# Performance work log

Measured on AMD Instinct MI355X. Metric: run time of the kernel, lower is better.

## Reference

```python
import jax, jax.numpy as jnp
import numpy as np

B, S, E, H, L = 2, 2048, 1024, 16, 64


def setup_inputs() -> dict:
    key = jax.random.key(0)
    ks = jax.random.split(key, 9)
    x = jax.random.normal(ks[0], (B, S, E), dtype=jnp.float32)
    # causal mask: 1 where attention allowed, 0 where blocked (mask==0 -> -inf)
    mask = jnp.tril(jnp.ones((1, S, S), dtype=jnp.int32))
    std = 0.02
    # per-head Linear weights stacked over heads; torch Linear stores W as [out, in]
    Wq = jax.random.normal(ks[1], (H, L, E), dtype=jnp.float32) * std
    Wk = jax.random.normal(ks[2], (H, L, E), dtype=jnp.float32) * std
    Wv = jax.random.normal(ks[3], (H, L, E), dtype=jnp.float32) * std
    bq = jax.random.normal(ks[4], (H, L), dtype=jnp.float32) * std
    bk = jax.random.normal(ks[5], (H, L), dtype=jnp.float32) * std
    bv = jax.random.normal(ks[6], (H, L), dtype=jnp.float32) * std
    Wo = jax.random.normal(ks[7], (E, H * L), dtype=jnp.float32) * std
    bo = jax.random.normal(ks[8], (E,), dtype=jnp.float32) * std
    return {"x": x, "mask": mask, "Wq": Wq, "bq": bq, "Wk": Wk, "bk": bk,
            "Wv": Wv, "bv": bv, "Wo": Wo, "bo": bo}


def reference(x, mask, Wq, bq, Wk, bk, Wv, bv, Wo, bo):
    # Q/K/V for all heads at once: [B, H, S, L]
    Q = jnp.einsum('bse,hle->bhsl', x, Wq) + bq[None, :, None, :]
    K = jnp.einsum('bse,hle->bhsl', x, Wk) + bk[None, :, None, :]
    V = jnp.einsum('bse,hle->bhsl', x, Wv) + bv[None, :, None, :]
    scale = jnp.sqrt(jnp.asarray(L, dtype=Q.dtype))
    scores = jnp.einsum('bhsl,bhtl->bhst', Q, K) / scale  # [B,H,S,S]
    scores = jnp.where(mask[:, None, :, :] == 0, -jnp.inf, scores)
    P = jax.nn.softmax(scores, axis=-1)
    O = jnp.einsum('bhst,bhtl->bhsl', P, V)  # [B,H,S,L]
    # concat heads along last dim (head order matches torch concat)
    z = jnp.transpose(O, (0, 2, 1, 3)).reshape(O.shape[0], O.shape[2], -1)
    return jnp.einsum('bsk,ek->bse', z, Wo) + bo
```

## Files before the change

### kernel.cpp

```cpp
#include <hip/hip_runtime.h>
#include <math.h>

typedef unsigned short US;
typedef __attribute__((ext_vector_type(8))) __bf16 bf16x8;
typedef __attribute__((ext_vector_type(4))) float f32x4;
typedef __attribute__((ext_vector_type(4))) unsigned short us4;

#define MFMA16(a, b, c) __builtin_amdgcn_mfma_f32_16x16x32_bf16(a, b, c, 0, 0, 0)

__device__ __forceinline__ US f2bf(float f) {
  union { float f; unsigned u; } v; v.f = f;
  unsigned r = v.u + 0x7fffu + ((v.u >> 16) & 1u);
  return (US)(r >> 16);
}
__device__ __forceinline__ float bf2f(US u) {
  union { unsigned u; float f; } v; v.u = ((unsigned)u) << 16; return v.f;
}

__device__ __forceinline__ void gload16(const void* g, void* l) {
  __builtin_amdgcn_global_load_lds(
      (const __attribute__((address_space(1))) unsigned int*)g,
      (__attribute__((address_space(3))) unsigned int*)l, 16, 0, 0);
}

__global__ __launch_bounds__(256) void convert_k(
    const float* __restrict__ x, const float* __restrict__ Wq,
    const float* __restrict__ Wk, const float* __restrict__ Wv,
    const float* __restrict__ Wo,
    US* __restrict__ xb, US* __restrict__ wqkv, US* __restrict__ wob) {
  long i = (long)blockIdx.x * blockDim.x + threadIdx.x;
  long e4 = i * 4;
  if (e4 >= 8388608L) return;
  const float* src; US* dst;
  if (e4 < 4194304L) { src = x + e4; dst = xb + e4; }
  else if (e4 < 7340032L) {
    long off = e4 - 4194304L;
    dst = wqkv + off;
    src = (off < 1048576L) ? Wq + off
        : (off < 2097152L ? Wk + (off - 1048576L) : Wv + (off - 2097152L));
  } else {
    long off = e4 - 7340032L;
    src = Wo + off; dst = wob + off;
  }
  float4 v = *(const float4*)src;
  us4 o; o.x = f2bf(v.x); o.y = f2bf(v.y); o.z = f2bf(v.z); o.w = f2bf(v.w);
  *(us4*)dst = o;
}

template <int MODE>
__global__ __launch_bounds__(256) void gemm128(
    const US* __restrict__ A, const US* __restrict__ BT,
    int K, int lda, int ldb, int N,
    const float* __restrict__ b0, const float* __restrict__ b1,
    const float* __restrict__ b2,
    US* __restrict__ oQ, US* __restrict__ oK, US* __restrict__ oV,
    float* __restrict__ oF) {
  __shared__ __align__(16) US As[128 * 32];
  __shared__ __align__(16) US Bs[128 * 32];
  const int tid = threadIdx.x, lane = tid & 63;
  const int w = tid >> 6, wr = w >> 1, wc = w & 1;
  const int m0 = blockIdx.x * 128, n0 = blockIdx.y * 128;
  f32x4 acc[4][4] = {};
  const int r0 = tid >> 2, c0 = (tid & 3) * 8;

  for (int kt = 0; kt < K; kt += 32) {
    gload16(A + (size_t)(m0 + r0) * lda + kt + c0, As + tid * 8);
    gload16(A + (size_t)(m0 + r0 + 64) * lda + kt + c0, As + (tid + 256) * 8);
    gload16(BT + (size_t)(n0 + r0) * ldb + kt + c0, Bs + tid * 8);
    gload16(BT + (size_t)(n0 + r0 + 64) * ldb + kt + c0, Bs + (tid + 256) * 8);
    __syncthreads();
    bf16x8 af[4], bfm[4];
#pragma unroll
    for (int i = 0; i < 4; ++i)
      af[i] = *(const bf16x8*)(As + (wr * 64 + i * 16 + (lane & 15)) * 32 + (lane >> 4) * 8);
#pragma unroll
    for (int j = 0; j < 4; ++j)
      bfm[j] = *(const bf16x8*)(Bs + (wc * 64 + j * 16 + (lane & 15)) * 32 + (lane >> 4) * 8);
#pragma unroll
    for (int i = 0; i < 4; ++i)
#pragma unroll
      for (int j = 0; j < 4; ++j)
        acc[i][j] = MFMA16(af[i], bfm[j], acc[i][j]);
    __syncthreads();
  }

#pragma unroll
  for (int i = 0; i < 4; ++i) {
#pragma unroll
    for (int j = 0; j < 4; ++j) {
#pragma unroll
      for (int r = 0; r < 4; ++r) {
        int m = m0 + wr * 64 + i * 16 + (lane >> 4) * 4 + r;
        int n = n0 + wc * 64 + j * 16 + (lane & 15);
        float v = acc[i][j][r];
        if (MODE == 0) {
          int bb = m >> 11, s = m & 2047;
          int sec = n >> 10, idx = n & 1023;
          int h = idx >> 6, l = idx & 63;
          size_t bhsl = (((size_t)bb * 16 + h) * 2048 + s) * 64 + l;
          if (sec == 0)      oQ[bhsl] = f2bf((v + b0[idx]) * 0.125f);
          else if (sec == 1) oK[bhsl] = f2bf(v + b1[idx]);
          else oV[(((size_t)bb * 16 + h) * 64 + l) * 2048 + s] = f2bf(v + b2[idx]);
        } else {
          oF[(size_t)m * N + n] = v + b0[n];
        }
      }
    }
  }
}

__global__ __launch_bounds__(256) void attn_k(
    const US* __restrict__ Qb, const US* __restrict__ Kb,
    const US* __restrict__ Vtb, US* __restrict__ opart,
    float2* __restrict__ mlpart) {
  __shared__ __align__(16) US Ks[64 * 64];
  __shared__ __align__(16) US Vs[64 * 64];
  __shared__ __align__(16) US Ps[4][16 * 72];
  const int tid = threadIdx.x, lane = tid & 63, w = tid >> 6;
  const int slot = blockIdx.x >> 6;
  const int qt = 31 - slot;
  const int bh = (blockIdx.x & 63) >> 1;
  const int half = blockIdx.x & 1;
  const int h0 = (qt + 2) >> 1;
  const int kstart = half ? h0 : 0;
  const int kend = half ? (qt + 1) : h0;
  const size_t pslot = (size_t)(bh * 32 + qt) * 2 + half;

  if (kstart >= kend) {
    US* op = opart + pslot * 4096;
    us4 z; z.x = 0; z.y = 0; z.z = 0; z.w = 0;
#pragma unroll
    for (int j = 0; j < 4; ++j) *(us4*)(op + tid * 16 + j * 4) = z;
    if ((lane >> 4) == 0)
      mlpart[pslot * 64 + w * 16 + lane] = make_float2(-INFINITY, 0.f);
    return;
  }

  const US* Qp = Qb + ((size_t)bh * 2048 + qt * 64) * 64;
  const char* Kbase = (const char*)(Kb + (size_t)bh * 2048 * 64);
  const char* Vbase = (const char*)(Vtb + (size_t)bh * 64 * 2048);

  const int row0 = tid >> 3, col16 = (tid & 7) * 16;
  const int row1 = row0 + 32;
  const int soff0 = (row0 * 128 + col16) ^ ((row0 & 7) << 4);
  const int soff1 = soff0 + 32 * 128;

  bf16x8 aq[2];
  {
    int qrow = w * 16 + (lane & 15);
#pragma unroll
    for (int kk = 0; kk < 2; ++kk)
      aq[kk] = *(const bf16x8*)(Qp + qrow * 64 + kk * 32 + (lane >> 4) * 8);
  }
  f32x4 o[4] = {};
  float m = -INFINITY, l = 0.f;

  int4 rk0, rk1, rv0, rv1;
#define LOADT(KT)                                                              \
  do {                                                                         \
    rk0 = *(const int4*)(Kbase + ((size_t)((KT)*64 + row0)) * 128 + col16);    \
    rk1 = *(const int4*)(Kbase + ((size_t)((KT)*64 + row1)) * 128 + col16);    \
    rv0 = *(const int4*)(Vbase + (size_t)row0 * 4096 + (KT)*128 + col16);      \
    rv1 = *(const int4*)(Vbase + (size_t)row1 * 4096 + (KT)*128 + col16);      \
  } while (0)
#define WRITET()                                                               \
  do {                                                                         \
    *(int4*)((char*)Ks + soff0) = rk0;                                         \
    *(int4*)((char*)Ks + soff1) = rk1;                                         \
    *(int4*)((char*)Vs + soff0) = rv0;                                         \
    *(int4*)((char*)Vs + soff1) = rv1;                                         \
  } while (0)

  LOADT(kstart);
  WRITET();
  __syncthreads();

  for (int kt = kstart; kt < kend; ++kt) {
    if (kt + 1 < kend) LOADT(kt + 1);

    f32x4 sc[4];
    __builtin_amdgcn_s_setprio(1);
#pragma unroll
    for (int nt = 0; nt < 4; ++nt) {
      f32x4 s = {0.f, 0.f, 0.f, 0.f};
#pragma unroll
      for (int kk = 0; kk < 2; ++kk) {
        int rr = nt * 16 + (lane & 15);
        int off = rr * 128 + kk * 64 + (lane >> 4) * 16;
        off ^= (rr & 7) << 4;
        bf16x8 bkf = *(const bf16x8*)((const char*)Ks + off);
        s = MFMA16(bkf, aq[kk], s);
      }
      sc[nt] = s;
    }
    __builtin_amdgcn_s_setprio(0);

    if (kt == qt) {
      int q_in = w * 16 + (lane & 15);
#pragma unroll
      for (int nt = 0; nt < 4; ++nt)
#pragma unroll
        for (int r = 0; r < 4; ++r) {
          int kv_in = nt * 16 + (lane >> 4) * 4 + r;
          if (kv_in > q_in) sc[nt][r] = -INFINITY;
        }
    }

    {
      float m01 = fmaxf(fmaxf(sc[0][0], sc[0][1]), fmaxf(sc[0][2], sc[0][3]));
      float m23 = fmaxf(fmaxf(sc[1][0], sc[1][1]), fmaxf(sc[1][2], sc[1][3]));
      float m45 = fmaxf(fmaxf(sc[2][0], sc[2][1]), fmaxf(sc[2][2], sc[2][3]));
      float m67 = fmaxf(fmaxf(sc[3][0], sc[3][1]), fmaxf(sc[3][2], sc[3][3]));
      float mx = fmaxf(fmaxf(m01, m23), fmaxf(m45, m67));
      mx = fmaxf(mx, __shfl_xor(mx, 16));
      mx = fmaxf(mx, __shfl_xor(mx, 32));
      float mnew = fmaxf(m, mx);
      float scale = __expf(m - mnew);
      m = mnew;
      float s0 = 0.f, s1 = 0.f, s2 = 0.f, s3 = 0.f;
#pragma unroll
      for (int nt = 0; nt < 4; ++nt) {
        float p0 = __expf(sc[nt][0] - m);
        float p1 = __expf(sc[nt][1] - m);
        float p2 = __expf(sc[nt][2] - m);
        float p3 = __expf(sc[nt][3] - m);
        sc[nt][0] = p0; sc[nt][1] = p1; sc[nt][2] = p2; sc[nt][3] = p3;
        s0 += p0; s1 += p1; s2 += p2; s3 += p3;
      }
      float ssum = (s0 + s1) + (s2 + s3);
      ssum += __shfl_xor(ssum, 16);
      ssum += __shfl_xor(ssum, 32);
      l = l * scale + ssum;
#pragma unroll
      for (int r = 0; r < 4; ++r) {
        float sr = __shfl(scale, ((lane >> 4) << 2) + r, 64);
        o[0][r] *= sr; o[1][r] *= sr; o[2][r] *= sr; o[3][r] *= sr;
      }
    }

    US* pp = &Ps[w][0];
    const int pbase = (lane & 15) * 72 + (lane >> 4) * 4;
#pragma unroll
    for (int nt = 0; nt < 4; ++nt) {
      us4 w4;
      w4.x = f2bf(sc[nt][0]); w4.y = f2bf(sc[nt][1]);
      w4.z = f2bf(sc[nt][2]); w4.w = f2bf(sc[nt][3]);
      *(us4*)(pp + pbase + nt * 16) = w4;
    }

    __builtin_amdgcn_s_setprio(1);
#pragma unroll
    for (int kk = 0; kk < 2; ++kk) {
      bf16x8 pa = *(const bf16x8*)(pp + (lane & 15) * 72 + kk * 32 + (lane >> 4) * 8);
#pragma unroll
      for (int nt = 0; nt < 4; ++nt) {
        int rr = nt * 16 + (lane & 15);
        int off = rr * 128 + kk * 64 + (lane >> 4) * 16;
        off ^= (rr & 7) << 4;
        bf16x8 bvf = *(const bf16x8*)((const char*)Vs + off);
        o[nt] = MFMA16(pa, bvf, o[nt]);
      }
    }
    __builtin_amdgcn_s_setprio(0);

    __syncthreads();
    if (kt + 1 < kend) {
      WRITET();
      __syncthreads();
    }
  }
#undef LOADT
#undef WRITET

  US* op = opart + pslot * 4096;
#pragma unroll
  for (int r = 0; r < 4; ++r) {
    int row = w * 16 + (lane >> 4) * 4 + r;
#pragma unroll
    for (int nt = 0; nt < 4; ++nt) {
      int d = nt * 16 + (lane & 15);
      op[row * 64 + d] = f2bf(o[nt][r]);
    }
  }
  if ((lane >> 4) == 0)
    mlpart[pslot * 64 + w * 16 + lane] = make_float2(m, l);
}

__global__ __launch_bounds__(256) void merge_k(
    const US* __restrict__ opart, const float2* __restrict__ mlpart,
    US* __restrict__ zb) {
  const int t = blockIdx.x;
  const int bh = t >> 5, qt = t & 31;
  const int b = bh >> 4, h = bh & 15;
  const int row = threadIdx.x >> 2;
  const int dg = (threadIdx.x & 3) * 16;
  const US* o1 = opart + ((size_t)t * 2 + 0) * 4096 + row * 64 + dg;
  const US* o2 = opart + ((size_t)t * 2 + 1) * 4096 + row * 64 + dg;
  float2 ml1 = mlpart[(t * 2 + 0) * 64 + row];
  float2 ml2 = mlpart[(t * 2 + 1) * 64 + row];
  float mm = fmaxf(ml1.x, ml2.x);
  float w1 = __expf(ml1.x - mm), w2 = __expf(ml2.x - mm);
  float li = 1.0f / (ml1.y * w1 + ml2.y * w2);
  w1 *= li; w2 *= li;
  int s = qt * 64 + row;
  US* dst = zb + ((size_t)b * 2048 + s) * 1024 + h * 64 + dg;
#pragma unroll
  for (int j = 0; j < 4; ++j) {
    us4 a = *(const us4*)(o1 + j * 4);
    us4 c = *(const us4*)(o2 + j * 4);
    us4 r;
    r.x = f2bf(bf2f(a.x) * w1 + bf2f(c.x) * w2);
    r.y = f2bf(bf2f(a.y) * w1 + bf2f(c.y) * w2);
    r.z = f2bf(bf2f(a.z) * w1 + bf2f(c.z) * w2);
    r.w = f2bf(bf2f(a.w) * w1 + bf2f(c.w) * w2);
    *(us4*)(dst + j * 4) = r;
  }
}

extern "C" void kernel_launch(void* const* d_in, const int* in_sizes, int n_in,
                              void* d_out, int out_size, void* d_ws, size_t ws_size,
                              hipStream_t stream) {
  (void)in_sizes; (void)n_in; (void)out_size; (void)ws_size;
  const float* x  = (const float*)d_in[0];
  const float* Wq = (const float*)d_in[2];
  const float* bq = (const float*)d_in[3];
  const float* Wk = (const float*)d_in[4];
  const float* bk = (const float*)d_in[5];
  const float* Wv = (const float*)d_in[6];
  const float* bv = (const float*)d_in[7];
  const float* Wo = (const float*)d_in[8];
  const float* bo = (const float*)d_in[9];
  char* ws = (char*)d_ws;
  US* xb     = (US*)(ws);
  float2* ml = (float2*)(ws);
  US* zb     = (US*)(ws + 1048576);
  US* wqkv   = (US*)(ws + 8388608);
  US* wob    = (US*)(ws + 14680064);
  US* Qb     = (US*)(ws + 16777216);
  US* Kb     = (US*)(ws + 25165824);
  US* Vtb    = (US*)(ws + 33554432);
  US* opart  = (US*)d_out;
  float* out = (float*)d_out;

  convert_k<<<dim3(8192), dim3(256), 0, stream>>>(x, Wq, Wk, Wv, Wo, xb, wqkv, wob);
  gemm128<0><<<dim3(32, 24), dim3(256), 0, stream>>>(
      xb, wqkv, 1024, 1024, 1024, 3072, bq, bk, bv, Qb, Kb, Vtb, (float*)nullptr);
  attn_k<<<dim3(2048), dim3(256), 0, stream>>>(Qb, Kb, Vtb, opart, ml);
  merge_k<<<dim3(1024), dim3(256), 0, stream>>>(opart, ml, zb);
  gemm128<1><<<dim3(32, 8), dim3(256), 0, stream>>>(
      zb, wob, 1024, 1024, 1024, 1024, bo, (const float*)nullptr, (const float*)nullptr,
      (US*)nullptr, (US*)nullptr, (US*)nullptr, out);
}
```

Baseline: 140.4 us.

## Double-buffer GEMM LDS tiles, swizzle blocks across XCDs, use exp2 softmax

The projection GEMMs now prefetch the next K tile into a second LDS buffer while computing on the current one, and remap a 1D grid so neighbouring tiles land on the same XCD for L2 reuse. Softmax folds log2(e) into the Q scaling and uses exp2f instead of __expf in attention and merge. The changes aim to hide global load latency, improve cache locality, and drop a multiply per exponential, at the cost of double the LDS per GEMM block.

```diff
diff --git a/kernel.cpp b/kernel.cpp
--- a/kernel.cpp
+++ b/kernel.cpp
@@ -50,39 +50,54 @@
 template <int MODE>
 __global__ __launch_bounds__(256) void gemm128(
     const US* __restrict__ A, const US* __restrict__ BT,
-    int K, int lda, int ldb, int N,
+    int K, int lda, int ldb, int N, int MT,
     const float* __restrict__ b0, const float* __restrict__ b1,
     const float* __restrict__ b2,
     US* __restrict__ oQ, US* __restrict__ oK, US* __restrict__ oV,
     float* __restrict__ oF) {
-  __shared__ __align__(16) US As[128 * 32];
-  __shared__ __align__(16) US Bs[128 * 32];
+  __shared__ __align__(16) US As[2][128 * 32];
+  __shared__ __align__(16) US Bs[2][128 * 32];
   const int tid = threadIdx.x, lane = tid & 63;
   const int w = tid >> 6, wr = w >> 1, wc = w & 1;
-  const int m0 = blockIdx.x * 128, n0 = blockIdx.y * 128;
+  const int cpx = gridDim.x >> 3;
+  const int swz = (blockIdx.x & 7) * cpx + (blockIdx.x >> 3);
+  const int m0 = (swz % MT) * 128, n0 = (swz / MT) * 128;
   f32x4 acc[4][4] = {};
   const int r0 = tid >> 2, c0 = (tid & 3) * 8;
 
+#define STAGE(B, KT)                                                           \
+  do {                                                                         \
+    gload16(A + (size_t)(m0 + r0) * lda + (KT) + c0, As[B] + tid * 8);         \
+    gload16(A + (size_t)(m0 + r0 + 64) * lda + (KT) + c0,                      \
+            As[B] + (tid + 256) * 8);                                          \
+    gload16(BT + (size_t)(n0 + r0) * ldb + (KT) + c0, Bs[B] + tid * 8);        \
+    gload16(BT + (size_t)(n0 + r0 + 64) * ldb + (KT) + c0,                     \
+            Bs[B] + (tid + 256) * 8);                                          \
+  } while (0)
+
+  STAGE(0, 0);
+  __syncthreads();
+  int cur = 0;
   for (int kt = 0; kt < K; kt += 32) {
-    gload16(A + (size_t)(m0 + r0) * lda + kt + c0, As + tid * 8);
-    gload16(A + (size_t)(m0 + r0 + 64) * lda + kt + c0, As + (tid + 256) * 8);
-    gload16(BT + (size_t)(n0 + r0) * ldb + kt + c0, Bs + tid * 8);
-    gload16(BT + (size_t)(n0 + r0 + 64) * ldb + kt + c0, Bs + (tid + 256) * 8);
-    __syncthreads();
+    if (kt + 32 < K) STAGE(cur ^ 1, kt + 32);
     bf16x8 af[4], bfm[4];
 #pragma unroll
     for (int i = 0; i < 4; ++i)
-      af[i] = *(const bf16x8*)(As + (wr * 64 + i * 16 + (lane & 15)) * 32 + (lane >> 4) * 8);
+      af[i] = *(const bf16x8*)(As[cur] + (wr * 64 + i * 16 + (lane & 15)) * 32 +
+                               (lane >> 4) * 8);
 #pragma unroll
     for (int j = 0; j < 4; ++j)
-      bfm[j] = *(const bf16x8*)(Bs + (wc * 64 + j * 16 + (lane & 15)) * 32 + (lane >> 4) * 8);
+      bfm[j] = *(const bf16x8*)(Bs[cur] + (wc * 64 + j * 16 + (lane & 15)) * 32 +
+                                (lane >> 4) * 8);
 #pragma unroll
     for (int i = 0; i < 4; ++i)
 #pragma unroll
       for (int j = 0; j < 4; ++j)
         acc[i][j] = MFMA16(af[i], bfm[j], acc[i][j]);
     __syncthreads();
-  }
+    cur ^= 1;
+  }
+#undef STAGE
 
 #pragma unroll
   for (int i = 0; i < 4; ++i) {
@@ -98,7 +113,7 @@
           int sec = n >> 10, idx = n & 1023;
           int h = idx >> 6, l = idx & 63;
           size_t bhsl = (((size_t)bb * 16 + h) * 2048 + s) * 64 + l;
-          if (sec == 0)      oQ[bhsl] = f2bf((v + b0[idx]) * 0.125f);
+          if (sec == 0)      oQ[bhsl] = f2bf((v + b0[idx]) * 0.18033688f);
           else if (sec == 1) oK[bhsl] = f2bf(v + b1[idx]);
           else oV[(((size_t)bb * 16 + h) * 64 + l) * 2048 + s] = f2bf(v + b2[idx]);
         } else {
@@ -215,15 +230,15 @@
       mx = fmaxf(mx, __shfl_xor(mx, 16));
       mx = fmaxf(mx, __shfl_xor(mx, 32));
       float mnew = fmaxf(m, mx);
-      float scale = __expf(m - mnew);
+      float scale = exp2f(m - mnew);
       m = mnew;
       float s0 = 0.f, s1 = 0.f, s2 = 0.f, s3 = 0.f;
 #pragma unroll
       for (int nt = 0; nt < 4; ++nt) {
-        float p0 = __expf(sc[nt][0] - m);
-        float p1 = __expf(sc[nt][1] - m);
-        float p2 = __expf(sc[nt][2] - m);
-        float p3 = __expf(sc[nt][3] - m);
+        float p0 = exp2f(sc[nt][0] - m);
+        float p1 = exp2f(sc[nt][1] - m);
+        float p2 = exp2f(sc[nt][2] - m);
+        float p3 = exp2f(sc[nt][3] - m);
         sc[nt][0] = p0; sc[nt][1] = p1; sc[nt][2] = p2; sc[nt][3] = p3;
         s0 += p0; s1 += p1; s2 += p2; s3 += p3;
       }
@@ -299,7 +314,7 @@
   float2 ml1 = mlpart[(t * 2 + 0) * 64 + row];
   float2 ml2 = mlpart[(t * 2 + 1) * 64 + row];
   float mm = fmaxf(ml1.x, ml2.x);
-  float w1 = __expf(ml1.x - mm), w2 = __expf(ml2.x - mm);
+  float w1 = exp2f(ml1.x - mm), w2 = exp2f(ml2.x - mm);
   float li = 1.0f / (ml1.y * w1 + ml2.y * w2);
   w1 *= li; w2 *= li;
   int s = qt * 64 + row;
@@ -343,11 +358,11 @@
   float* out = (float*)d_out;
 
   convert_k<<<dim3(8192), dim3(256), 0, stream>>>(x, Wq, Wk, Wv, Wo, xb, wqkv, wob);
-  gemm128<0><<<dim3(32, 24), dim3(256), 0, stream>>>(
-      xb, wqkv, 1024, 1024, 1024, 3072, bq, bk, bv, Qb, Kb, Vtb, (float*)nullptr);
+  gemm128<0><<<dim3(768), dim3(256), 0, stream>>>(
+      xb, wqkv, 1024, 1024, 1024, 3072, 32, bq, bk, bv, Qb, Kb, Vtb, (float*)nullptr);
   attn_k<<<dim3(2048), dim3(256), 0, stream>>>(Qb, Kb, Vtb, opart, ml);
   merge_k<<<dim3(1024), dim3(256), 0, stream>>>(opart, ml, zb);
-  gemm128<1><<<dim3(32, 8), dim3(256), 0, stream>>>(
-      zb, wob, 1024, 1024, 1024, 1024, bo, (const float*)nullptr, (const float*)nullptr,
+  gemm128<1><<<dim3(256), dim3(256), 0, stream>>>(
+      zb, wob, 1024, 1024, 1024, 1024, 32, bo, (const float*)nullptr, (const float*)nullptr,
       (US*)nullptr, (US*)nullptr, (US*)nullptr, out);
 }
```

Measured after the change: 140.7 us. Within noise of the previous version (+0.3%).
